# Performance work log

Measured on AMD Instinct MI355X. Metric: run time of the kernel, lower is better.

Reference implementation:

```python
import jax, jax.numpy as jnp
import numpy as np

N_NODES = 100000
N_EDGES = 1600000
IN_FEATS = 256
OUT_FEATS = 128


def setup_inputs() -> dict:
    key = jax.random.key(0)
    k1, k2, k3, k4 = jax.random.split(key, 4)
    feat = jax.random.normal(k1, (N_NODES, IN_FEATS), dtype=jnp.float32)
    src = jax.random.randint(k2, (N_EDGES,), 0, N_NODES, dtype=jnp.int64)
    dst = jax.random.randint(k3, (N_EDGES,), 0, N_NODES, dtype=jnp.int64)
    W = jax.random.normal(k4, (IN_FEATS, OUT_FEATS), dtype=jnp.float32) * (1.0 / np.sqrt(IN_FEATS))
    b = jnp.zeros((OUT_FEATS,), dtype=jnp.float32)
    return {"feat": feat, "src": src, "dst": dst, "W": W, "b": b}


def reference(feat, src, dst, W, b):
    # norm = 'both': symmetric degree normalization, clip degrees at 1
    ones = jnp.ones((src.shape[0],), dtype=jnp.float32)
    out_deg = jax.ops.segment_sum(ones, src, num_segments=N_NODES)  # out-degree per src node
    in_deg = jax.ops.segment_sum(ones, dst, num_segments=N_NODES)   # in-degree per dst node
    norm_src = jnp.power(jnp.clip(out_deg, 1.0, None), -0.5)[:, None]  # (N,1)
    norm_dst = jnp.power(jnp.clip(in_deg, 1.0, None), -0.5)[:, None]   # (N,1)

    h = feat * norm_src
    # in_feats (256) > out_feats (128): apply W before aggregation
    h = h @ W  # (N, out_feats)
    # copy_src + sum aggregation over edges (SpMM)
    msgs = h[src]  # (E, out_feats)
    rst = jax.ops.segment_sum(msgs, dst, num_segments=N_NODES)  # (N, out_feats)
    rst = rst * norm_dst
    rst = rst + b
    return rst
```

## Files before the change

### kernel.cpp

```cpp
#include <hip/hip_runtime.h>
#include <hip/hip_bf16.h>
#include <cstddef>

#define NN 100000
#define NE 1600000
#define INF 256
#define OUTF 128
#define NBKT 196
#define BSH 9
#define P1B 250
#define EPB 6400
#define SCL (NBKT * P1B)
#define SCLP 49152
#define P2CAP 10240

typedef __bf16 bf16x8 __attribute__((ext_vector_type(8)));
typedef float f32x4 __attribute__((ext_vector_type(4)));

__device__ __forceinline__ float bflo(uint v) { return __uint_as_float(v << 16); }
__device__ __forceinline__ float bfhi(uint v) { return __uint_as_float(v & 0xffff0000u); }

__global__ __launch_bounds__(256) void k_p1a(const int* __restrict__ src,
                                             const int* __restrict__ dst,
                                             int* __restrict__ ghd,
                                             int* __restrict__ ghs,
                                             const float* __restrict__ W,
                                             __bf16* __restrict__ Wt) {
  if (blockIdx.x >= P1B) {
    int i = (blockIdx.x - P1B) * 256 + threadIdx.x;
    if (i < SCLP - SCL) { ghd[SCL + i] = 0; ghs[SCL + i] = 0; }
    int n = i & 127, k = i >> 7;
    Wt[n * INF + k] = (__bf16)W[k * OUTF + n];
    return;
  }
  __shared__ int lhd[NBKT], lhs[NBKT];
  const int t = threadIdx.x;
  if (t < NBKT) { lhd[t] = 0; lhs[t] = 0; }
  __syncthreads();
  const int base = blockIdx.x * EPB;
#pragma unroll
  for (int i = 0; i < EPB / 256; ++i) {
    int e = base + i * 256 + t;
    atomicAdd(&lhd[dst[e] >> BSH], 1);
    atomicAdd(&lhs[src[e] >> BSH], 1);
  }
  __syncthreads();
  if (t < NBKT) {
    ghd[t * P1B + blockIdx.x] = lhd[t];
    ghs[t * P1B + blockIdx.x] = lhs[t];
  }
}

__global__ __launch_bounds__(1024) void k_p1b(int* __restrict__ ghd,
                                              int* __restrict__ ghs,
                                              int* __restrict__ row_start) {
  int* a = blockIdx.x ? ghs : ghd;
  __shared__ int wsum[16];
  const int t = threadIdx.x;
  const int lane = t & 63, wid = t >> 6;
  int4 v[12];
  const int4* p = (const int4*)(a + t * 48);
#pragma unroll
  for (int i = 0; i < 12; ++i) v[i] = p[i];
  int s = 0;
#pragma unroll
  for (int i = 0; i < 12; ++i) s += v[i].x + v[i].y + v[i].z + v[i].w;
  const int mysum = s;
#pragma unroll
  for (int d = 1; d < 64; d <<= 1) {
    int u = __shfl_up(s, d);
    if (lane >= d) s += u;
  }
  if (lane == 63) wsum[wid] = s;
  __syncthreads();
  if (wid == 0) {
    int ws = (lane < 16) ? wsum[lane] : 0;
    int inc = ws;
#pragma unroll
    for (int d = 1; d < 16; d <<= 1) {
      int u = __shfl_up(inc, d);
      if (lane >= d) inc += u;
    }
    if (lane < 16) wsum[lane] = inc - ws;
  }
  __syncthreads();
  int ex = wsum[wid] + s - mysum;
#pragma unroll
  for (int i = 0; i < 12; ++i) {
    int4 w;
    w.x = ex; ex += v[i].x;
    w.y = ex; ex += v[i].y;
    w.z = ex; ex += v[i].z;
    w.w = ex; ex += v[i].w;
    ((int4*)(a + t * 48))[i] = w;
  }
  if (blockIdx.x == 0 && t == 0) row_start[NN] = NE;
}

__global__ __launch_bounds__(256) void k_p1c(const int* __restrict__ src,
                                             const int* __restrict__ dst,
                                             const int* __restrict__ ghd,
                                             const int* __restrict__ ghs,
                                             uint* __restrict__ rec_d,
                                             ushort* __restrict__ rec_s) {
  __shared__ int hist[256];
  __shared__ int off[NBKT];
  __shared__ int adj[NBKT];
  __shared__ int sc[256];
  __shared__ uint d4[EPB];
  __shared__ unsigned char bkt[EPB];
  const int t = threadIdx.x;
  const int base = blockIdx.x * EPB;

  hist[t] = 0;
  __syncthreads();
#pragma unroll
  for (int i = 0; i < EPB / 256; ++i)
    atomicAdd(&hist[dst[base + i * 256 + t] >> BSH], 1);
  __syncthreads();
  int hv = hist[t];
  sc[t] = hv;
  __syncthreads();
  for (int o = 1; o < 256; o <<= 1) {
    int add = (t >= o) ? sc[t - o] : 0;
    __syncthreads();
    sc[t] += add;
    __syncthreads();
  }
  int lstart = sc[t] - hv;
  if (t < NBKT) {
    off[t] = lstart;
    adj[t] = ghd[t * P1B + blockIdx.x] - lstart;
  }
  __syncthreads();
#pragma unroll
  for (int i = 0; i < EPB / 256; ++i) {
    int e = base + i * 256 + t;
    int s = src[e], d = dst[e];
    int b = d >> BSH;
    int p = atomicAdd(&off[b], 1);
    d4[p] = ((uint)s << BSH) | (uint)(d & 511);
    bkt[p] = (unsigned char)b;
  }
  __syncthreads();
#pragma unroll
  for (int i = 0; i < EPB / 256; ++i) {
    int idx = i * 256 + t;
    rec_d[adj[bkt[idx]] + idx] = d4[idx];
  }
  __syncthreads();

  hist[t] = 0;
  __syncthreads();
#pragma unroll
  for (int i = 0; i < EPB / 256; ++i)
    atomicAdd(&hist[src[base + i * 256 + t] >> BSH], 1);
  __syncthreads();
  hv = hist[t];
  sc[t] = hv;
  __syncthreads();
  for (int o = 1; o < 256; o <<= 1) {
    int add = (t >= o) ? sc[t - o] : 0;
    __syncthreads();
    sc[t] += add;
    __syncthreads();
  }
  lstart = sc[t] - hv;
  if (t < NBKT) {
    off[t] = lstart;
    adj[t] = ghs[t * P1B + blockIdx.x] - lstart;
  }
  __syncthreads();
  ushort* s2 = (ushort*)d4;
#pragma unroll
  for (int i = 0; i < EPB / 256; ++i) {
    int s = src[base + i * 256 + t];
    int b = s >> BSH;
    int p = atomicAdd(&off[b], 1);
    s2[p] = (ushort)(s & 511);
    bkt[p] = (unsigned char)b;
  }
  __syncthreads();
#pragma unroll
  for (int i = 0; i < EPB / 256; ++i) {
    int idx = i * 256 + t;
    rec_s[adj[bkt[idx]] + idx] = s2[idx];
  }
}

__global__ __launch_bounds__(256) void k_p2(const int* __restrict__ ghd,
                                            const int* __restrict__ ghs,
                                            const uint* __restrict__ rec_d,
                                            const ushort* __restrict__ rec_s,
                                            int* __restrict__ edge_src,
                                            int* __restrict__ row_start,
                                            float* __restrict__ ns) {
  __shared__ int lh[512];
  __shared__ int sc[256];
  __shared__ int lbuf[P2CAP];
  const int k = blockIdx.x, t = threadIdx.x;
  {
    const int base = ghd[k * P1B];
    const int end = (k == NBKT - 1) ? NE : ghd[(k + 1) * P1B];
    const int cnt = end - base;
    lh[t] = 0; lh[t + 256] = 0;
    __syncthreads();
    for (int j = base + t; j < end; j += 256) atomicAdd(&lh[rec_d[j] & 511], 1);
    __syncthreads();
    int a0 = lh[2 * t], a1 = lh[2 * t + 1];
    sc[t] = a0 + a1;
    __syncthreads();
    for (int off = 1; off < 256; off <<= 1) {
      int add = (t >= off) ? sc[t - off] : 0;
      __syncthreads();
      sc[t] += add;
      __syncthreads();
    }
    int ex = t ? sc[t - 1] : 0;
    int e0 = ex, e1 = ex + a0;
    int n0 = k * 512 + 2 * t;
    if (n0 < NN) row_start[n0] = base + e0;
    if (n0 + 1 < NN) row_start[n0 + 1] = base + e1;
    __syncthreads();
    lh[2 * t] = e0;
    lh[2 * t + 1] = e1;
    __syncthreads();
    if (cnt <= P2CAP) {
      for (int j = base + t; j < end; j += 256) {
        uint r = rec_d[j];
        int p = atomicAdd(&lh[r & 511], 1);
        lbuf[p] = (int)(r >> BSH);
      }
      __syncthreads();
      for (int i = t; i < cnt; i += 256)
        edge_src[base + i] = lbuf[i];
    } else {
      for (int j = base + t; j < end; j += 256) {
        uint r = rec_d[j];
        int p = atomicAdd(&lh[r & 511], 1);
        edge_src[base + p] = (int)(r >> BSH);
      }
    }
  }
  __syncthreads();
  {
    const int base = ghs[k * P1B];
    const int end = (k == NBKT - 1) ? NE : ghs[(k + 1) * P1B];
    lh[t] = 0; lh[t + 256] = 0;
    __syncthreads();
    for (int j = base + t; j < end; j += 256) atomicAdd(&lh[rec_s[j]], 1);
    __syncthreads();
    int n0 = k * 512 + t, n1 = n0 + 256;
    if (n0 < NN) { int c = lh[t];       ns[n0] = rsqrtf((float)(c > 1 ? c : 1)); }
    if (n1 < NN) { int c = lh[t + 256]; ns[n1] = rsqrtf((float)(c > 1 ? c : 1)); }
  }
}

__global__ __launch_bounds__(512, 4) void k_gemm(const float* __restrict__ feat,
                                                 const __bf16* __restrict__ Wt,
                                                 const float* __restrict__ ns,
                                                 __bf16* __restrict__ h) {
  __shared__ __attribute__((aligned(16))) char lB[65536];
  const int tid = threadIdx.x;
  const int w = tid >> 6, l = tid & 63;
  const int lr = l & 15, kg = l >> 4;
  const int row0 = blockIdx.x * 128 + w * 16;

#pragma unroll
  for (int i = 0; i < 8; ++i) {
    int c = i * 512 + tid;
    int col = c >> 5, g = c & 31;
    bf16x8 v = *(const bf16x8*)(Wt + (size_t)col * INF + g * 8);
    *(bf16x8*)(lB + col * 512 + ((g ^ (col & 7)) * 16)) = v;
  }
  __syncthreads();

  int r0 = row0 + lr; if (r0 >= NN) r0 = NN - 1;
  const float4* ap4k = (const float4*)(feat + (size_t)r0 * INF) + kg * 2;

  f32x4 acc[8];
#pragma unroll
  for (int j = 0; j < 8; ++j) acc[j] = (f32x4)0.0f;

  const char* bb = lB + lr * 512;
  const int lx = lr & 7;

  float4 buf0[4], buf1[4];
#pragma unroll
  for (int i = 0; i < 4; ++i) {
    buf0[i] = ap4k[i * 8];
    buf1[i] = ap4k[i * 8 + 1];
  }
#pragma unroll
  for (int kk = 0; kk < 8; ++kk) {
    float4 c0 = buf0[kk & 3], c1 = buf1[kk & 3];
    if (kk < 4) {
      buf0[kk & 3] = ap4k[(kk + 4) * 8];
      buf1[kk & 3] = ap4k[(kk + 4) * 8 + 1];
    }
    bf16x8 a;
#pragma unroll
    for (int j = 0; j < 4; ++j) {
      a[j] = (__bf16)c0[j];
      a[4 + j] = (__bf16)c1[j];
    }
#pragma unroll
    for (int nf = 0; nf < 8; ++nf) {
      bf16x8 b = *(const bf16x8*)(bb + nf * 8192 + (((kk * 4 + kg) ^ lx) * 16));
      acc[nf] = __builtin_amdgcn_mfma_f32_16x16x32_bf16(a, b, acc[nf], 0, 0, 0);
    }
  }

#pragma unroll
  for (int r = 0; r < 4; ++r) {
    int row = row0 + kg * 4 + r;
    if (row < NN) {
      float nsv = ns[row];
      __bf16* hp = h + (size_t)row * OUTF + lr;
#pragma unroll
      for (int nf = 0; nf < 8; ++nf)
        hp[nf * 16] = (__bf16)(acc[nf][r] * nsv);
    }
  }
}

__global__ __launch_bounds__(256) void k_aggr(const uint4* __restrict__ h4,
                                              const int* __restrict__ row_start,
                                              const int* __restrict__ edge_src,
                                              const float* __restrict__ bias,
                                              float* __restrict__ out) {
  const int wave = threadIdx.x >> 6;
  const int lane = threadIdx.x & 63;
  const int q = lane >> 4;
  const int cl = lane & 15;
  const int n = blockIdx.x * 4 + wave;
  const int s0 = row_start[n];
  const int s1 = row_start[n + 1];
  const int cnt = s1 - s0;

  float a0 = 0.f, a1 = 0.f, a2 = 0.f, a3 = 0.f, a4 = 0.f, a5 = 0.f, a6 = 0.f, a7 = 0.f;
  for (int j0 = 0; j0 < cnt; j0 += 64) {
    int nb = cnt - j0; if (nb > 64) nb = 64;
    int idv = 0;
    if (lane < nb) idv = edge_src[s0 + j0 + lane];
#pragma unroll 8
    for (int j = 0; j < nb; j += 4) {
      int jj = j + q;
      int e = __shfl(idv, jj);
      if (jj < nb) {
        uint4 v = h4[(size_t)e * 16 + cl];
        a0 += bflo(v.x); a1 += bfhi(v.x);
        a2 += bflo(v.y); a3 += bfhi(v.y);
        a4 += bflo(v.z); a5 += bfhi(v.z);
        a6 += bflo(v.w); a7 += bfhi(v.w);
      }
    }
  }
  a0 += __shfl_xor(a0, 16); a1 += __shfl_xor(a1, 16); a2 += __shfl_xor(a2, 16); a3 += __shfl_xor(a3, 16);
  a4 += __shfl_xor(a4, 16); a5 += __shfl_xor(a5, 16); a6 += __shfl_xor(a6, 16); a7 += __shfl_xor(a7, 16);
  a0 += __shfl_xor(a0, 32); a1 += __shfl_xor(a1, 32); a2 += __shfl_xor(a2, 32); a3 += __shfl_xor(a3, 32);
  a4 += __shfl_xor(a4, 32); a5 += __shfl_xor(a5, 32); a6 += __shfl_xor(a6, 32); a7 += __shfl_xor(a7, 32);

  if (q == 0) {
    float ndv = rsqrtf((float)(cnt > 1 ? cnt : 1));
    const float4* b4 = (const float4*)bias;
    float4 ba = b4[2 * cl], bb = b4[2 * cl + 1];
    float4 o0, o1;
    o0.x = a0 * ndv + ba.x; o0.y = a1 * ndv + ba.y; o0.z = a2 * ndv + ba.z; o0.w = a3 * ndv + ba.w;
    o1.x = a4 * ndv + bb.x; o1.y = a5 * ndv + bb.y; o1.z = a6 * ndv + bb.z; o1.w = a7 * ndv + bb.w;
    float4* op = (float4*)(out + (size_t)n * OUTF);
    op[2 * cl] = o0;
    op[2 * cl + 1] = o1;
  }
}

extern "C" void kernel_launch(void* const* d_in, const int* in_sizes, int n_in,
                              void* d_out, int out_size, void* d_ws, size_t ws_size,
                              hipStream_t stream) {
  const float* feat = (const float*)d_in[0];
  const int* src = (const int*)d_in[1];
  const int* dst = (const int*)d_in[2];
  const float* Wm = (const float*)d_in[3];
  const float* bias = (const float*)d_in[4];
  float* out = (float*)d_out;

  char* ws = (char*)d_ws;
  __bf16* h        = (__bf16*)(ws + 0);
  __bf16* Wt       = (__bf16*)(ws + 25600000);
  int*    ghd      = (int*)(ws + 25665536);
  int*    ghs      = (int*)(ws + 25862144);
  uint*   rec_d    = (uint*)(ws + 26058752);
  ushort* rec_s    = (ushort*)(ws + 32458752);
  int*    edge_src = (int*)(ws + 35658752);
  int*    row_start= (int*)(ws + 42058752);
  float*  ns       = (float*)(ws + 42458768);

  k_p1a<<<P1B + 128, 256, 0, stream>>>(src, dst, ghd, ghs, Wm, Wt);
  k_p1b<<<2, 1024, 0, stream>>>(ghd, ghs, row_start);
  k_p1c<<<P1B, 256, 0, stream>>>(src, dst, ghd, ghs, rec_d, rec_s);
  k_p2<<<NBKT, 256, 0, stream>>>(ghd, ghs, rec_d, rec_s, edge_src, row_start, ns);
  k_gemm<<<(NN + 127) / 128, 512, 0, stream>>>(feat, Wt, ns, h);
  k_aggr<<<NN / 4, 256, 0, stream>>>((const uint4*)h, row_start, edge_src, bias, out);
}
```

Measured before the change: 165.1 us.

## Fuse GEMM with histogram kernel and move source normalization into aggregation

The dense feature GEMM now runs in the same launch as the edge bucket histogram, and it converts W to bf16 straight into shared memory. This removes the Wt transpose pass and one kernel launch, and lets the GEMM overlap with the histogram and sort phases. Because the GEMM now runs before the source-degree norm is known, the norm is applied per edge in the aggregation kernel. That adds an extra gather of ns per edge and a multiply per element there. The GEMM blocks also each re-read and convert the full fp32 W.

```diff
diff --git a/kernel.cpp b/kernel.cpp
--- a/kernel.cpp
+++ b/kernel.cpp
@@ -13,6 +13,7 @@
 #define SCL (NBKT * P1B)
 #define SCLP 49152
 #define P2CAP 10240
+#define NGB 782
 
 typedef __bf16 bf16x8 __attribute__((ext_vector_type(8)));
 typedef float f32x4 __attribute__((ext_vector_type(4)));
@@ -20,34 +21,102 @@
 __device__ __forceinline__ float bflo(uint v) { return __uint_as_float(v << 16); }
 __device__ __forceinline__ float bfhi(uint v) { return __uint_as_float(v & 0xffff0000u); }
 
-__global__ __launch_bounds__(256) void k_p1a(const int* __restrict__ src,
+__global__ __launch_bounds__(512, 4) void k1(const float* __restrict__ feat,
+                                             const float* __restrict__ Wm,
+                                             __bf16* __restrict__ h,
+                                             const int* __restrict__ src,
                                              const int* __restrict__ dst,
                                              int* __restrict__ ghd,
-                                             int* __restrict__ ghs,
-                                             const float* __restrict__ W,
-                                             __bf16* __restrict__ Wt) {
-  if (blockIdx.x >= P1B) {
-    int i = (blockIdx.x - P1B) * 256 + threadIdx.x;
-    if (i < SCLP - SCL) { ghd[SCL + i] = 0; ghs[SCL + i] = 0; }
-    int n = i & 127, k = i >> 7;
-    Wt[n * INF + k] = (__bf16)W[k * OUTF + n];
+                                             int* __restrict__ ghs) {
+  __shared__ __attribute__((aligned(16))) char lmem[65536];
+  const int tid = threadIdx.x;
+
+  if (blockIdx.x >= NGB) {
+    const int b = blockIdx.x - NGB;
+    int* lhd = (int*)lmem;
+    int* lhs = ((int*)lmem) + 256;
+    if (b == 0 && tid < SCLP - SCL) { ghd[SCL + tid] = 0; ghs[SCL + tid] = 0; }
+    if (tid < NBKT) { lhd[tid] = 0; lhs[tid] = 0; }
+    __syncthreads();
+    const int base = b * EPB;
+    for (int e = base + tid; e < base + EPB; e += 512) {
+      atomicAdd(&lhd[dst[e] >> BSH], 1);
+      atomicAdd(&lhs[src[e] >> BSH], 1);
+    }
+    __syncthreads();
+    if (tid < NBKT) {
+      ghd[tid * P1B + b] = lhd[tid];
+      ghs[tid * P1B + b] = lhs[tid];
+    }
     return;
   }
-  __shared__ int lhd[NBKT], lhs[NBKT];
-  const int t = threadIdx.x;
-  if (t < NBKT) { lhd[t] = 0; lhs[t] = 0; }
-  __syncthreads();
-  const int base = blockIdx.x * EPB;
-#pragma unroll
-  for (int i = 0; i < EPB / 256; ++i) {
-    int e = base + i * 256 + t;
-    atomicAdd(&lhd[dst[e] >> BSH], 1);
-    atomicAdd(&lhs[src[e] >> BSH], 1);
-  }
-  __syncthreads();
-  if (t < NBKT) {
-    ghd[t * P1B + blockIdx.x] = lhd[t];
-    ghs[t * P1B + blockIdx.x] = lhs[t];
+
+  char* lB = lmem;
+  const int w = tid >> 6, l = tid & 63;
+  const int lr = l & 15, kg = l >> 4;
+  const int row0 = blockIdx.x * 128 + w * 16;
+
+  {
+    const float4* W4 = (const float4*)Wm;
+#pragma unroll
+    for (int i = 0; i < 8; ++i) {
+      int c = i * 512 + tid;
+      int k = c >> 4, n0 = (c & 15) << 3;
+      float4 f0 = W4[c * 2], f1 = W4[c * 2 + 1];
+      int g = k >> 3, kb = (k & 7) * 2;
+      float ff[8] = {f0.x, f0.y, f0.z, f0.w, f1.x, f1.y, f1.z, f1.w};
+#pragma unroll
+      for (int j = 0; j < 8; ++j)
+        *(__bf16*)(lB + (n0 + j) * 512 + ((g ^ j) * 16) + kb) = (__bf16)ff[j];
+    }
+  }
+  __syncthreads();
+
+  int r0 = row0 + lr; if (r0 >= NN) r0 = NN - 1;
+  const float4* ap4k = (const float4*)(feat + (size_t)r0 * INF) + kg * 2;
+
+  f32x4 acc[8];
+#pragma unroll
+  for (int j = 0; j < 8; ++j) acc[j] = (f32x4)0.0f;
+
+  const char* bb = lB + lr * 512;
+  const int lx = lr & 7;
+
+  float4 buf0[4], buf1[4];
+#pragma unroll
+  for (int i = 0; i < 4; ++i) {
+    buf0[i] = ap4k[i * 8];
+    buf1[i] = ap4k[i * 8 + 1];
+  }
+#pragma unroll
+  for (int kk = 0; kk < 8; ++kk) {
+    float4 c0 = buf0[kk & 3], c1 = buf1[kk & 3];
+    if (kk < 4) {
+      buf0[kk & 3] = ap4k[(kk + 4) * 8];
+      buf1[kk & 3] = ap4k[(kk + 4) * 8 + 1];
+    }
+    bf16x8 a;
+#pragma unroll
+    for (int j = 0; j < 4; ++j) {
+      a[j] = (__bf16)c0[j];
+      a[4 + j] = (__bf16)c1[j];
+    }
+#pragma unroll
+    for (int nf = 0; nf < 8; ++nf) {
+      bf16x8 b = *(const bf16x8*)(bb + nf * 8192 + (((kk * 4 + kg) ^ lx) * 16));
+      acc[nf] = __builtin_amdgcn_mfma_f32_16x16x32_bf16(a, b, acc[nf], 0, 0, 0);
+    }
+  }
+
+#pragma unroll
+  for (int r = 0; r < 4; ++r) {
+    int row = row0 + kg * 4 + r;
+    if (row < NN) {
+      __bf16* hp = h + (size_t)row * OUTF + lr;
+#pragma unroll
+      for (int nf = 0; nf < 8; ++nf)
+        hp[nf * 16] = (__bf16)(acc[nf][r]);
+    }
   }
 }
 
@@ -256,76 +325,9 @@
   }
 }
 
-__global__ __launch_bounds__(512, 4) void k_gemm(const float* __restrict__ feat,
-                                                 const __bf16* __restrict__ Wt,
-                                                 const float* __restrict__ ns,
-                                                 __bf16* __restrict__ h) {
-  __shared__ __attribute__((aligned(16))) char lB[65536];
-  const int tid = threadIdx.x;
-  const int w = tid >> 6, l = tid & 63;
-  const int lr = l & 15, kg = l >> 4;
-  const int row0 = blockIdx.x * 128 + w * 16;
-
-#pragma unroll
-  for (int i = 0; i < 8; ++i) {
-    int c = i * 512 + tid;
-    int col = c >> 5, g = c & 31;
-    bf16x8 v = *(const bf16x8*)(Wt + (size_t)col * INF + g * 8);
-    *(bf16x8*)(lB + col * 512 + ((g ^ (col & 7)) * 16)) = v;
-  }
-  __syncthreads();
-
-  int r0 = row0 + lr; if (r0 >= NN) r0 = NN - 1;
-  const float4* ap4k = (const float4*)(feat + (size_t)r0 * INF) + kg * 2;
-
-  f32x4 acc[8];
-#pragma unroll
-  for (int j = 0; j < 8; ++j) acc[j] = (f32x4)0.0f;
-
-  const char* bb = lB + lr * 512;
-  const int lx = lr & 7;
-
-  float4 buf0[4], buf1[4];
-#pragma unroll
-  for (int i = 0; i < 4; ++i) {
-    buf0[i] = ap4k[i * 8];
-    buf1[i] = ap4k[i * 8 + 1];
-  }
-#pragma unroll
-  for (int kk = 0; kk < 8; ++kk) {
-    float4 c0 = buf0[kk & 3], c1 = buf1[kk & 3];
-    if (kk < 4) {
-      buf0[kk & 3] = ap4k[(kk + 4) * 8];
-      buf1[kk & 3] = ap4k[(kk + 4) * 8 + 1];
-    }
-    bf16x8 a;
-#pragma unroll
-    for (int j = 0; j < 4; ++j) {
-      a[j] = (__bf16)c0[j];
-      a[4 + j] = (__bf16)c1[j];
-    }
-#pragma unroll
-    for (int nf = 0; nf < 8; ++nf) {
-      bf16x8 b = *(const bf16x8*)(bb + nf * 8192 + (((kk * 4 + kg) ^ lx) * 16));
-      acc[nf] = __builtin_amdgcn_mfma_f32_16x16x32_bf16(a, b, acc[nf], 0, 0, 0);
-    }
-  }
-
-#pragma unroll
-  for (int r = 0; r < 4; ++r) {
-    int row = row0 + kg * 4 + r;
-    if (row < NN) {
-      float nsv = ns[row];
-      __bf16* hp = h + (size_t)row * OUTF + lr;
-#pragma unroll
-      for (int nf = 0; nf < 8; ++nf)
-        hp[nf * 16] = (__bf16)(acc[nf][r] * nsv);
-    }
-  }
-}
-
 __global__ __launch_bounds__(256) void k_aggr(const uint4* __restrict__ h4,
                                               const int* __restrict__ row_start,
+                                              const float* __restrict__ ns,
                                               const int* __restrict__ edge_src,
                                               const float* __restrict__ bias,
                                               float* __restrict__ out) {
@@ -341,18 +343,19 @@
   float a0 = 0.f, a1 = 0.f, a2 = 0.f, a3 = 0.f, a4 = 0.f, a5 = 0.f, a6 = 0.f, a7 = 0.f;
   for (int j0 = 0; j0 < cnt; j0 += 64) {
     int nb = cnt - j0; if (nb > 64) nb = 64;
-    int idv = 0;
-    if (lane < nb) idv = edge_src[s0 + j0 + lane];
+    int idv = 0; float nsv = 0.f;
+    if (lane < nb) { idv = edge_src[s0 + j0 + lane]; nsv = ns[idv]; }
 #pragma unroll 8
     for (int j = 0; j < nb; j += 4) {
       int jj = j + q;
       int e = __shfl(idv, jj);
+      float w2 = __shfl(nsv, jj);
       if (jj < nb) {
         uint4 v = h4[(size_t)e * 16 + cl];
-        a0 += bflo(v.x); a1 += bfhi(v.x);
-        a2 += bflo(v.y); a3 += bfhi(v.y);
-        a4 += bflo(v.z); a5 += bfhi(v.z);
-        a6 += bflo(v.w); a7 += bfhi(v.w);
+        a0 += w2 * bflo(v.x); a1 += w2 * bfhi(v.x);
+        a2 += w2 * bflo(v.y); a3 += w2 * bfhi(v.y);
+        a4 += w2 * bflo(v.z); a5 += w2 * bfhi(v.z);
+        a6 += w2 * bflo(v.w); a7 += w2 * bfhi(v.w);
       }
     }
   }
@@ -386,7 +389,6 @@
 
   char* ws = (char*)d_ws;
   __bf16* h        = (__bf16*)(ws + 0);
-  __bf16* Wt       = (__bf16*)(ws + 25600000);
   int*    ghd      = (int*)(ws + 25665536);
   int*    ghs      = (int*)(ws + 25862144);
   uint*   rec_d    = (uint*)(ws + 26058752);
@@ -395,10 +397,9 @@
   int*    row_start= (int*)(ws + 42058752);
   float*  ns       = (float*)(ws + 42458768);
 
-  k_p1a<<<P1B + 128, 256, 0, stream>>>(src, dst, ghd, ghs, Wm, Wt);
+  k1<<<NGB + P1B, 512, 0, stream>>>(feat, Wm, h, src, dst, ghd, ghs);
   k_p1b<<<2, 1024, 0, stream>>>(ghd, ghs, row_start);
   k_p1c<<<P1B, 256, 0, stream>>>(src, dst, ghd, ghs, rec_d, rec_s);
   k_p2<<<NBKT, 256, 0, stream>>>(ghd, ghs, rec_d, rec_s, edge_src, row_start, ns);
-  k_gemm<<<(NN + 127) / 128, 512, 0, stream>>>(feat, Wt, ns, h);
-  k_aggr<<<NN / 4, 256, 0, stream>>>((const uint4*)h, row_start, edge_src, bias, out);
-}
+  k_aggr<<<NN / 4, 256, 0, stream>>>((const uint4*)h, row_start, ns, edge_src, bias, out);
+}
```

Result: slower. 176.0 us (+6.6%).
